# Optimization experiments

Hardware: AMD Instinct MI355X
Metric: run time of the kernel (lower is better)

The kernel has to match this reference:

```python
import jax, jax.numpy as jnp
import numpy as np

N_NODES = 500000
N_EDGES = 16000000


def setup_inputs() -> dict:
    key = jax.random.key(0)
    k1, k2, k3, k4, k5, k6, k7 = jax.random.split(key, 7)
    x = jax.random.normal(k1, (N_NODES, 2), dtype=jnp.float32)
    edge_index = jax.random.randint(k2, (2, N_EDGES), 0, N_NODES, dtype=jnp.int64)
    edge_weight = jax.random.uniform(k3, (N_EDGES,), dtype=jnp.float32)
    # GCNConv linear weights (PyG stores weight [in, out] for x @ W) + bias
    W1 = jax.random.normal(k4, (2, 8), dtype=jnp.float32) * (1.0 / np.sqrt(2.0))
    b1 = jnp.zeros((8,), dtype=jnp.float32)
    W2 = jax.random.normal(k5, (8, 2), dtype=jnp.float32) * (1.0 / np.sqrt(8.0))
    b2 = jnp.zeros((2,), dtype=jnp.float32)
    return {"x": x, "edge_index": edge_index, "edge_weight": edge_weight,
            "W1": W1, "b1": b1, "W2": W2, "b2": b2}


def _gcn_norm(edge_index, edge_weight, num_nodes):
    # PyG gcn_norm: add self-loops (fill=1), symmetric D^-1/2 A D^-1/2
    loop = jnp.arange(num_nodes, dtype=edge_index.dtype)
    src = jnp.concatenate([edge_index[0], loop])
    dst = jnp.concatenate([edge_index[1], loop])
    w = jnp.concatenate([edge_weight, jnp.ones((num_nodes,), edge_weight.dtype)])
    deg = jax.ops.segment_sum(w, dst, num_segments=num_nodes)
    dinv = jnp.where(deg > 0, jax.lax.rsqrt(jnp.where(deg > 0, deg, 1.0)), 0.0)
    norm = dinv[src] * w * dinv[dst]
    return src, dst, norm


def _gcn_layer(x, src, dst, norm, W, b, num_nodes):
    h = x @ W                      # [N, out]
    msg = h[src] * norm[:, None]   # gather + edge scale, [E+N, out]
    out = jax.ops.segment_sum(msg, dst, num_segments=num_nodes)  # scatter-add
    return out + b


def reference(x, edge_index, edge_weight, W1, b1, W2, b2):
    n = x.shape[0]
    src, dst, norm = _gcn_norm(edge_index, edge_weight, n)
    h = _gcn_layer(x, src, dst, norm, W1, b1, n)
    h = jax.nn.relu(h)
    h = _gcn_layer(h, src, dst, norm, W2, b2, n)
    return jax.nn.softmax(h, axis=1)
```

## Files before the change

kernel.cpp:

```cpp
#include <hip/hip_runtime.h>
#include <math.h>

#define NNODES 500000
#define NEDGES 16000000
#define NBINS 512
#define BINSHIFT 10
#define BINMASK 1023
#define CB 512
#define NT 256


#define OFF_FLAG   0
#define OFF_BASE   64
#define OFF_TOT    1024
#define OFF_COUNTS 2048
#define OFF_OFFS   264192
#define OFF_DEGREP 526336
#define OFF_DINV   1526336
#define OFF_AGG1   2026336
#define OFF_AGG2   4026336
#define OFF_H2     6026336
#define OFF_REC    7026336
#define WS_NEED_FAST (((size_t)OFF_REC + 2ull * NEDGES) * 4ull)

__device__ __forceinline__ void atomAddF(float* p, float v) {
    unsafeAtomicAdd(p, v);
}

__device__ __forceinline__ int clampIdx(int i) {
    return ((unsigned)i < (unsigned)NNODES) ? i : 0;
}

template <bool I64>
__device__ __forceinline__ int4 loadIdx4(const int* __restrict__ p, int i) {
    if (!I64) {
        return ((const int4*)p)[i];
    } else {
        const longlong2* q = (const longlong2*)p;
        longlong2 a = q[2 * i];
        longlong2 b = q[2 * i + 1];
        return make_int4((int)a.x, (int)a.y, (int)b.x, (int)b.y);
    }
}

__global__ __launch_bounds__(256) void k_detect(
        const int* __restrict__ ei, int* __restrict__ flag) {
    __shared__ int any_nz;
    if (threadIdx.x == 0) any_nz = 0;
    __syncthreads();
    int nz = 0;
    const int SAMPLES = 1024;
    const int step = NEDGES / SAMPLES;
    for (int t = threadIdx.x; t < SAMPLES; t += blockDim.x) {
        int k = t * step;
        nz |= (ei[2 * k + 1] != 0);
    }
    if (nz) atomicOr(&any_nz, 1);
    __syncthreads();
    if (threadIdx.x == 0) flag[0] = any_nz ? 0 : 1;
}


template <bool I64>
__device__ __forceinline__ void count_body(
        const int* __restrict__ dstb, unsigned* __restrict__ counts) {
    __shared__ unsigned hist[NBINS];
    for (int j = threadIdx.x; j < NBINS; j += NT) hist[j] = 0;
    __syncthreads();
    const int Q = NEDGES / 4;
    const int qpb = (Q + CB - 1) / CB;
    int q0 = blockIdx.x * qpb, q1 = min(q0 + qpb, Q);
    for (int i = q0 + threadIdx.x; i < q1; i += NT) {
        int4 d = loadIdx4<I64>(dstb, i);
        atomicAdd(&hist[clampIdx(d.x) >> BINSHIFT], 1u);
        atomicAdd(&hist[clampIdx(d.y) >> BINSHIFT], 1u);
        atomicAdd(&hist[clampIdx(d.z) >> BINSHIFT], 1u);
        atomicAdd(&hist[clampIdx(d.w) >> BINSHIFT], 1u);
    }
    __syncthreads();
    for (int j = threadIdx.x; j < NBINS; j += NT)
        counts[(size_t)j * CB + blockIdx.x] = hist[j];
}

__global__ __launch_bounds__(256) void kb_count(
        const int* __restrict__ ei, const int* __restrict__ flag,
        unsigned* __restrict__ counts) {
    if (flag[0]) count_body<true >(ei + 2 * (size_t)NEDGES, counts);
    else         count_body<false>(ei + (size_t)NEDGES,     counts);
}

__global__ __launch_bounds__(256) void kb_tot(
        const unsigned* __restrict__ counts, unsigned* __restrict__ tot) {
    int b = blockIdx.x, t = threadIdx.x;
    __shared__ unsigned r[NT];
    r[t] = counts[(size_t)b * CB + t] + counts[(size_t)b * CB + t + 256];
    __syncthreads();
    for (int d = NT / 2; d > 0; d >>= 1) {
        if (t < d) r[t] += r[t + d];
        __syncthreads();
    }
    if (t == 0) tot[b] = r[0];
}

__global__ __launch_bounds__(256) void kb_scanbase(
        const unsigned* __restrict__ tot, unsigned* __restrict__ base) {
    __shared__ unsigned sc[NBINS];
    int t = threadIdx.x;
    unsigned o0 = tot[t], o1 = tot[t + 256];
    sc[t] = o0; sc[t + 256] = o1;
    __syncthreads();
    for (int d = 1; d < NBINS; d <<= 1) {
        unsigned a0 = (t >= d) ? sc[t - d] : 0u;
        unsigned a1 = (t + 256 >= d) ? sc[t + 256 - d] : 0u;
        __syncthreads();
        sc[t] += a0; sc[t + 256] += a1;
        __syncthreads();
    }
    base[t] = sc[t] - o0;
    base[t + 256] = sc[t + 256] - o1;
    if (t == 255) base[NBINS] = sc[NBINS - 1];
}

__global__ __launch_bounds__(256) void kb_offsets(
        const unsigned* __restrict__ counts, const unsigned* __restrict__ base,
        unsigned* __restrict__ offs) {
    int b = blockIdx.x, t = threadIdx.x;
    __shared__ unsigned sc[CB];
    unsigned o0 = counts[(size_t)b * CB + t], o1 = counts[(size_t)b * CB + t + 256];
    sc[t] = o0; sc[t + 256] = o1;
    __syncthreads();
    for (int d = 1; d < CB; d <<= 1) {
        unsigned a0 = (t >= d) ? sc[t - d] : 0u;
        unsigned a1 = (t + 256 >= d) ? sc[t + 256 - d] : 0u;
        __syncthreads();
        sc[t] += a0; sc[t + 256] += a1;
        __syncthreads();
    }
    unsigned bb = base[b];
    offs[(size_t)b * CB + t]       = bb + sc[t] - o0;
    offs[(size_t)b * CB + t + 256] = bb + sc[t + 256] - o1;
}

template <bool I64>
__device__ __forceinline__ void scatter_body(
        const int* __restrict__ srcb, const int* __restrict__ dstb,
        const float* __restrict__ ew, const unsigned* __restrict__ offs,
        uint2* __restrict__ rec) {
    __shared__ unsigned cur[NBINS];
    for (int j = threadIdx.x; j < NBINS; j += NT)
        cur[j] = offs[(size_t)j * CB + blockIdx.x];
    __syncthreads();
    const int Q = NEDGES / 4;
    const int qpb = (Q + CB - 1) / CB;
    int q0 = blockIdx.x * qpb, q1 = min(q0 + qpb, Q);
    for (int i = q0 + threadIdx.x; i < q1; i += NT) {
        int4   s = loadIdx4<I64>(srcb, i);
        int4   d = loadIdx4<I64>(dstb, i);
        float4 w = ((const float4*)ew)[i];
        int sv[4] = {clampIdx(s.x), clampIdx(s.y), clampIdx(s.z), clampIdx(s.w)};
        int dv[4] = {clampIdx(d.x), clampIdx(d.y), clampIdx(d.z), clampIdx(d.w)};
        float wv[4] = {w.x, w.y, w.z, w.w};
#pragma unroll
        for (int k = 0; k < 4; ++k) {
            int bin = dv[k] >> BINSHIFT;
            unsigned slot = atomicAdd(&cur[bin], 1u);
            unsigned key = ((unsigned)(dv[k] & BINMASK) << 19) | (unsigned)sv[k];
            rec[slot] = make_uint2(key, __float_as_uint(wv[k]));
        }
    }
}

__global__ __launch_bounds__(256) void kb_scatter(
        const int* __restrict__ ei, const int* __restrict__ flag,
        const float* __restrict__ ew, const unsigned* __restrict__ offs,
        uint2* __restrict__ rec) {
    if (flag[0]) scatter_body<true >(ei, ei + 2 * (size_t)NEDGES, ew, offs, rec);
    else         scatter_body<false>(ei, ei + (size_t)NEDGES,     ew, offs, rec);
}

__global__ __launch_bounds__(256) void kb_degree(
        const uint2* __restrict__ rec, const unsigned* __restrict__ base,
        float* __restrict__ degrep) {
    int bin = blockIdx.x >> 1, half = blockIdx.x & 1, t = threadIdx.x;
    __shared__ float sdeg[1024];
    for (int j = t; j < 1024; j += NT) sdeg[j] = 0.f;
    __syncthreads();
    int s = base[bin], e = base[bin + 1];
    int len = e - s, h = len >> 1;
    int b0 = s + (half ? h : 0);
    int b1 = half ? e : s + h;
    for (int i = b0 + t; i < b1; i += NT) {
        uint2 r = rec[i];
        atomAddF(&sdeg[r.x >> 19], __uint_as_float(r.y));
    }
    __syncthreads();
    int nodebase = bin << BINSHIFT;
    for (int j = t; j < 1024; j += NT) {
        int node = nodebase + j;
        if (node < NNODES) degrep[(size_t)half * NNODES + node] = sdeg[j];
    }
}

__global__ __launch_bounds__(256) void kb_dinv(
        const float* __restrict__ degrep, float* __restrict__ dinv, int N) {
    int i = blockIdx.x * blockDim.x + threadIdx.x;
    if (i >= N) return;
    dinv[i] = rsqrtf(degrep[i] + degrep[(size_t)N + i] + 1.0f);
}

__global__ __launch_bounds__(256) void kb_agg(
        const uint2* __restrict__ rec, const unsigned* __restrict__ base,
        const float* __restrict__ dinv, const float2* __restrict__ feat,
        float2* __restrict__ outrep) {
    int bin = blockIdx.x >> 1, half = blockIdx.x & 1, t = threadIdx.x;
    __shared__ float sagg[2048];
    __shared__ float sdinv[1024];
    for (int j = t; j < 2048; j += NT) sagg[j] = 0.f;
    int nodebase = bin << BINSHIFT;
    for (int j = t; j < 1024; j += NT) {
        int node = nodebase + j;
        sdinv[j] = (node < NNODES) ? dinv[node] : 0.f;
    }
    __syncthreads();
    int s = base[bin], e = base[bin + 1];
    int len = e - s, h = len >> 1;
    int b0 = s + (half ? h : 0);
    int b1 = half ? e : s + h;
    for (int i = b0 + t; i < b1; i += NT) {
        uint2 r = rec[i];
        int dl  = r.x >> 19;
        int src = r.x & 0x7FFFF;
        float nrm = dinv[src] * __uint_as_float(r.y) * sdinv[dl];
        float2 f = feat[src];
        atomAddF(&sagg[2 * dl],     f.x * nrm);
        atomAddF(&sagg[2 * dl + 1], f.y * nrm);
    }
    __syncthreads();
    for (int j = t; j < 1024; j += NT) {
        int node = nodebase + j;
        if (node < NNODES)
            outrep[(size_t)half * NNODES + node] = make_float2(sagg[2 * j], sagg[2 * j + 1]);
    }
}

__global__ __launch_bounds__(256) void kb_mid(
        const float2* __restrict__ aggrep, const float2* __restrict__ x,
        const float* __restrict__ dinv, const float* __restrict__ W1,
        const float* __restrict__ b1, const float* __restrict__ W2,
        float2* __restrict__ h2, int N) {
    int i = blockIdx.x * blockDim.x + threadIdx.x;
    if (i >= N) return;
    float s = dinv[i], s2 = s * s;
    float2 a0 = aggrep[i], a1 = aggrep[(size_t)N + i];
    float2 xa = x[i];
    float vx = a0.x + a1.x + xa.x * s2;
    float vy = a0.y + a1.y + xa.y * s2;
    float o0 = 0.f, o1 = 0.f;
#pragma unroll
    for (int j = 0; j < 8; ++j) {
        float tt = fmaf(vx, W1[j], fmaf(vy, W1[8 + j], b1[j]));
        tt = fmaxf(tt, 0.0f);
        o0 = fmaf(tt, W2[2 * j],     o0);
        o1 = fmaf(tt, W2[2 * j + 1], o1);
    }
    h2[i] = make_float2(o0, o1);
}

__global__ __launch_bounds__(256) void kb_fin(
        const float2* __restrict__ aggrep, const float2* __restrict__ h2,
        const float* __restrict__ dinv, const float* __restrict__ b2,
        float2* __restrict__ out, int N) {
    int i = blockIdx.x * blockDim.x + threadIdx.x;
    if (i >= N) return;
    float s = dinv[i], s2 = s * s;
    float2 a0 = aggrep[i], a1 = aggrep[(size_t)N + i];
    float2 h = h2[i];
    float o0 = a0.x + a1.x + h.x * s2 + b2[0];
    float o1 = a0.y + a1.y + h.y * s2 + b2[1];
    float m  = fmaxf(o0, o1);
    float e0 = expf(o0 - m), e1 = expf(o1 - m);
    float inv = 1.0f / (e0 + e1);
    out[i] = make_float2(e0 * inv, e1 * inv);
}


__global__ __launch_bounds__(256) void k_zero(float4* __restrict__ p, int n4) {
    int stride = gridDim.x * blockDim.x;
    for (int i = blockIdx.x * blockDim.x + threadIdx.x; i < n4; i += stride)
        p[i] = make_float4(0.f, 0.f, 0.f, 0.f);
}

template <bool I64>
__device__ __forceinline__ void degree_body(
        const int* __restrict__ dst, const float* __restrict__ ew,
        float* __restrict__ deg, int Q) {
    int stride = gridDim.x * blockDim.x;
    for (int i = blockIdx.x * blockDim.x + threadIdx.x; i < Q; i += stride) {
        int4   d = loadIdx4<I64>(dst, i);
        float4 w = ((const float4*)ew)[i];
        atomAddF(&deg[clampIdx(d.x)], w.x);
        atomAddF(&deg[clampIdx(d.y)], w.y);
        atomAddF(&deg[clampIdx(d.z)], w.z);
        atomAddF(&deg[clampIdx(d.w)], w.w);
    }
}

__global__ __launch_bounds__(256) void k_degree(
        const int* __restrict__ ei, const int* __restrict__ flag,
        const float* __restrict__ ew, float* __restrict__ deg, int Q) {
    if (flag[0]) degree_body<true >(ei + 2 * (size_t)NEDGES, ew, deg, Q);
    else         degree_body<false>(ei + (size_t)NEDGES,     ew, deg, Q);
}

__global__ __launch_bounds__(256) void k_dinv(float* __restrict__ deg, int N) {
    int i = blockIdx.x * blockDim.x + threadIdx.x;
    if (i >= N) return;
    deg[i] = rsqrtf(deg[i] + 1.0f);
}

template <bool I64>
__device__ __forceinline__ void edge_body(
        const int* __restrict__ src, const int* __restrict__ dst,
        const float* __restrict__ ew, const float* __restrict__ dinv,
        const float* __restrict__ feat, float* __restrict__ agg, int Q) {
    int stride = gridDim.x * blockDim.x;
    for (int i = blockIdx.x * blockDim.x + threadIdx.x; i < Q; i += stride) {
        int4   s = loadIdx4<I64>(src, i);
        int4   d = loadIdx4<I64>(dst, i);
        float4 w = ((const float4*)ew)[i];
        s.x = clampIdx(s.x); s.y = clampIdx(s.y);
        s.z = clampIdx(s.z); s.w = clampIdx(s.w);
        d.x = clampIdx(d.x); d.y = clampIdx(d.y);
        d.z = clampIdx(d.z); d.w = clampIdx(d.w);
        float n0 = dinv[s.x] * w.x * dinv[d.x];
        float n1 = dinv[s.y] * w.y * dinv[d.y];
        float n2 = dinv[s.z] * w.z * dinv[d.z];
        float n3 = dinv[s.w] * w.w * dinv[d.w];
        float2 f0 = ((const float2*)feat)[s.x];
        float2 f1 = ((const float2*)feat)[s.y];
        float2 f2 = ((const float2*)feat)[s.z];
        float2 f3 = ((const float2*)feat)[s.w];
        float* o0 = agg + 2 * (size_t)d.x;
        float* o1 = agg + 2 * (size_t)d.y;
        float* o2 = agg + 2 * (size_t)d.z;
        float* o3 = agg + 2 * (size_t)d.w;
        atomAddF(o0,     f0.x * n0);
        atomAddF(o0 + 1, f0.y * n0);
        atomAddF(o1,     f1.x * n1);
        atomAddF(o1 + 1, f1.y * n1);
        atomAddF(o2,     f2.x * n2);
        atomAddF(o2 + 1, f2.y * n2);
        atomAddF(o3,     f3.x * n3);
        atomAddF(o3 + 1, f3.y * n3);
    }
}

__global__ __launch_bounds__(256) void k_edge(
        const int* __restrict__ ei, const int* __restrict__ flag,
        const float* __restrict__ ew, const float* __restrict__ dinv,
        const float* __restrict__ feat, float* __restrict__ agg, int Q) {
    if (flag[0]) edge_body<true >(ei, ei + 2 * (size_t)NEDGES, ew, dinv, feat, agg, Q);
    else         edge_body<false>(ei, ei + (size_t)NEDGES,     ew, dinv, feat, agg, Q);
}

__global__ __launch_bounds__(256) void k_mid(
        const float* __restrict__ aggX, const float* __restrict__ x,
        const float* __restrict__ dinv, const float* __restrict__ W1,
        const float* __restrict__ b1, const float* __restrict__ W2,
        float* __restrict__ h2, int N) {
    int i = blockIdx.x * blockDim.x + threadIdx.x;
    if (i >= N) return;
    float s = dinv[i], s2 = s * s;
    float2 xa = ((const float2*)x)[i];
    float2 ag = ((const float2*)aggX)[i];
    float vx = ag.x + xa.x * s2;
    float vy = ag.y + xa.y * s2;
    float o0 = 0.f, o1 = 0.f;
#pragma unroll
    for (int j = 0; j < 8; ++j) {
        float t = fmaf(vx, W1[j], fmaf(vy, W1[8 + j], b1[j]));
        t = fmaxf(t, 0.0f);
        o0 = fmaf(t, W2[2 * j],     o0);
        o1 = fmaf(t, W2[2 * j + 1], o1);
    }
    ((float2*)h2)[i] = make_float2(o0, o1);
}

__global__ __launch_bounds__(256) void k_fin(
        const float* __restrict__ agg2, const float* __restrict__ h2,
        const float* __restrict__ dinv, const float* __restrict__ b2,
        float* __restrict__ out, int N) {
    int i = blockIdx.x * blockDim.x + threadIdx.x;
    if (i >= N) return;
    float s = dinv[i], s2 = s * s;
    float2 a = ((const float2*)agg2)[i];
    float2 h = ((const float2*)h2)[i];
    float o0 = a.x + h.x * s2 + b2[0];
    float o1 = a.y + h.y * s2 + b2[1];
    float m  = fmaxf(o0, o1);
    float e0 = expf(o0 - m), e1 = expf(o1 - m);
    float inv = 1.0f / (e0 + e1);
    ((float2*)out)[i] = make_float2(e0 * inv, e1 * inv);
}


extern "C" void kernel_launch(void* const* d_in, const int* in_sizes, int n_in,
                              void* d_out, int out_size, void* d_ws, size_t ws_size,
                              hipStream_t stream) {
    const float* x  = (const float*)d_in[0];
    const int*   ei = (const int*)d_in[1];
    const float* ew = (const float*)d_in[2];
    const float* W1 = (const float*)d_in[3];
    const float* b1 = (const float*)d_in[4];
    const float* W2 = (const float*)d_in[5];
    const float* b2 = (const float*)d_in[6];
    float* out = (float*)d_out;
    unsigned* wsu = (unsigned*)d_ws;
    float*    wsf = (float*)d_ws;

    const int N = NNODES, E = NEDGES, Q = E / 4;
    const int NB = (N + NT - 1) / NT;
    int* flag = (int*)(wsu + OFF_FLAG);

    bool fast = ws_size >= WS_NEED_FAST;

    k_detect<<<1, NT, 0, stream>>>(ei, flag);

    if (fast) {
        unsigned* base   = wsu + OFF_BASE;
        unsigned* tot    = wsu + OFF_TOT;
        unsigned* counts = wsu + OFF_COUNTS;
        unsigned* offs   = wsu + OFF_OFFS;
        float*    degrep = wsf + OFF_DEGREP;
        float*    dinv   = wsf + OFF_DINV;
        float2*   agg1   = (float2*)(wsf + OFF_AGG1);
        float2*   agg2   = (float2*)(wsf + OFF_AGG2);
        float2*   h2     = (float2*)(wsf + OFF_H2);
        uint2*    rec    = (uint2*)(wsu + OFF_REC);

        kb_count   <<<CB,        NT, 0, stream>>>(ei, flag, counts);
        kb_tot     <<<NBINS,     NT, 0, stream>>>(counts, tot);
        kb_scanbase<<<1,         NT, 0, stream>>>(tot, base);
        kb_offsets <<<NBINS,     NT, 0, stream>>>(counts, base, offs);
        kb_scatter <<<CB,        NT, 0, stream>>>(ei, flag, ew, offs, rec);
        kb_degree  <<<2 * NBINS, NT, 0, stream>>>(rec, base, degrep);
        kb_dinv    <<<NB,        NT, 0, stream>>>(degrep, dinv, N);
        kb_agg     <<<2 * NBINS, NT, 0, stream>>>(rec, base, dinv, (const float2*)x, agg1);
        kb_mid     <<<NB,        NT, 0, stream>>>(agg1, (const float2*)x, dinv, W1, b1, W2, h2, N);
        kb_agg     <<<2 * NBINS, NT, 0, stream>>>(rec, base, dinv, (const float2*)h2, agg2);
        kb_fin     <<<NB,        NT, 0, stream>>>(agg2, h2, dinv, b2, (float2*)out, N);
    } else {
        float* deg  = wsf + 64;
        float* aggX = wsf + 64 + (size_t)N;
        float* agg2 = wsf + 64 + (size_t)3 * N;
        float* h2   = wsf + 64 + (size_t)5 * N;
        const int EB = 2048;
        const int ZB = ((5 * N / 4) + NT - 1) / NT;

        k_zero  <<<ZB, NT, 0, stream>>>((float4*)deg, 5 * N / 4);
        k_degree<<<EB, NT, 0, stream>>>(ei, flag, ew, deg, Q);
        k_dinv  <<<NB, NT, 0, stream>>>(deg, N);
        k_edge  <<<EB, NT, 0, stream>>>(ei, flag, ew, deg, x, aggX, Q);
        k_mid   <<<NB, NT, 0, stream>>>(aggX, x, deg, W1, b1, W2, h2, N);
        k_edge  <<<EB, NT, 0, stream>>>(ei, flag, ew, deg, h2, agg2, Q);
        k_fin   <<<NB, NT, 0, stream>>>(agg2, h2, deg, b2, out, N);
    }
}
```

Before: 921.0 us.

## Use larger destination bins, four-way replication, and non-temporal edge loads

Destination bins grow from 1024 to 2048 nodes, giving 256 bins, with 1024 count blocks. Each bin is now split across four replica blocks instead of two, and the count and offset matrices are stored block-major, which changes the scan kernels. The destination dinv factor moves out of the per-edge loop into the mid and final kernels, and edge streams use non-temporal loads. The aim is more parallel blocks per bin, fewer per-edge multiplies, and less cache pollution, at the cost of twice the replica partial buffers to read and reduce per node.

```diff
diff --git a/kernel.cpp b/kernel.cpp
--- a/kernel.cpp
+++ b/kernel.cpp
@@ -3,10 +3,11 @@
 
 #define NNODES 500000
 #define NEDGES 16000000
-#define NBINS 512
-#define BINSHIFT 10
-#define BINMASK 1023
-#define CB 512
+#define NBINS 256
+#define BINSHIFT 11
+#define BINMASK 2047
+#define CB 1024
+#define REP 4
 #define NT 256
 
 
@@ -16,12 +17,15 @@
 #define OFF_COUNTS 2048
 #define OFF_OFFS   264192
 #define OFF_DEGREP 526336
-#define OFF_DINV   1526336
-#define OFF_AGG1   2026336
-#define OFF_AGG2   4026336
-#define OFF_H2     6026336
+#define OFF_H2     526336
+#define OFF_DINV   2526336
+#define OFF_AGG    3026336
 #define OFF_REC    7026336
 #define WS_NEED_FAST (((size_t)OFF_REC + 2ull * NEDGES) * 4ull)
+
+typedef int       i32x4 __attribute__((ext_vector_type(4)));
+typedef float     f32x4 __attribute__((ext_vector_type(4)));
+typedef long long i64x2 __attribute__((ext_vector_type(2)));
 
 __device__ __forceinline__ void atomAddF(float* p, float v) {
     unsafeAtomicAdd(p, v);
@@ -43,6 +47,23 @@
     }
 }
 
+template <bool I64>
+__device__ __forceinline__ int4 loadIdx4NT(const int* __restrict__ p, int i) {
+    if (!I64) {
+        i32x4 v = __builtin_nontemporal_load(((const i32x4*)p) + i);
+        return make_int4(v.x, v.y, v.z, v.w);
+    } else {
+        i64x2 a = __builtin_nontemporal_load(((const i64x2*)p) + 2 * i);
+        i64x2 b = __builtin_nontemporal_load(((const i64x2*)p) + 2 * i + 1);
+        return make_int4((int)a.x, (int)a.y, (int)b.x, (int)b.y);
+    }
+}
+
+__device__ __forceinline__ float4 loadF4NT(const float* __restrict__ p, int i) {
+    f32x4 v = __builtin_nontemporal_load(((const f32x4*)p) + i);
+    return make_float4(v.x, v.y, v.z, v.w);
+}
+
 __global__ __launch_bounds__(256) void k_detect(
         const int* __restrict__ ei, int* __restrict__ flag) {
     __shared__ int any_nz;
@@ -71,7 +92,7 @@
     const int qpb = (Q + CB - 1) / CB;
     int q0 = blockIdx.x * qpb, q1 = min(q0 + qpb, Q);
     for (int i = q0 + threadIdx.x; i < q1; i += NT) {
-        int4 d = loadIdx4<I64>(dstb, i);
+        int4 d = loadIdx4NT<I64>(dstb, i);
         atomicAdd(&hist[clampIdx(d.x) >> BINSHIFT], 1u);
         atomicAdd(&hist[clampIdx(d.y) >> BINSHIFT], 1u);
         atomicAdd(&hist[clampIdx(d.z) >> BINSHIFT], 1u);
@@ -79,7 +100,7 @@
     }
     __syncthreads();
     for (int j = threadIdx.x; j < NBINS; j += NT)
-        counts[(size_t)j * CB + blockIdx.x] = hist[j];
+        counts[(size_t)blockIdx.x * NBINS + j] = hist[j];
 }
 
 __global__ __launch_bounds__(256) void kb_count(
@@ -91,54 +112,65 @@
 
 __global__ __launch_bounds__(256) void kb_tot(
         const unsigned* __restrict__ counts, unsigned* __restrict__ tot) {
-    int b = blockIdx.x, t = threadIdx.x;
+    int j = blockIdx.x, t = threadIdx.x;
     __shared__ unsigned r[NT];
-    r[t] = counts[(size_t)b * CB + t] + counts[(size_t)b * CB + t + 256];
+    unsigned s = 0;
+#pragma unroll
+    for (int k = 0; k < CB / NT; ++k)
+        s += counts[(size_t)(t * (CB / NT) + k) * NBINS + j];
+    r[t] = s;
     __syncthreads();
     for (int d = NT / 2; d > 0; d >>= 1) {
         if (t < d) r[t] += r[t + d];
         __syncthreads();
     }
-    if (t == 0) tot[b] = r[0];
+    if (t == 0) tot[j] = r[0];
 }
 
 __global__ __launch_bounds__(256) void kb_scanbase(
         const unsigned* __restrict__ tot, unsigned* __restrict__ base) {
     __shared__ unsigned sc[NBINS];
     int t = threadIdx.x;
-    unsigned o0 = tot[t], o1 = tot[t + 256];
-    sc[t] = o0; sc[t + 256] = o1;
+    unsigned o = tot[t];
+    sc[t] = o;
     __syncthreads();
     for (int d = 1; d < NBINS; d <<= 1) {
-        unsigned a0 = (t >= d) ? sc[t - d] : 0u;
-        unsigned a1 = (t + 256 >= d) ? sc[t + 256 - d] : 0u;
+        unsigned a = (t >= d) ? sc[t - d] : 0u;
         __syncthreads();
-        sc[t] += a0; sc[t + 256] += a1;
+        sc[t] += a;
         __syncthreads();
     }
-    base[t] = sc[t] - o0;
-    base[t + 256] = sc[t + 256] - o1;
-    if (t == 255) base[NBINS] = sc[NBINS - 1];
+    base[t] = sc[t] - o;
+    if (t == NBINS - 1) base[NBINS] = sc[NBINS - 1];
 }
 
 __global__ __launch_bounds__(256) void kb_offsets(
         const unsigned* __restrict__ counts, const unsigned* __restrict__ base,
         unsigned* __restrict__ offs) {
-    int b = blockIdx.x, t = threadIdx.x;
-    __shared__ unsigned sc[CB];
-    unsigned o0 = counts[(size_t)b * CB + t], o1 = counts[(size_t)b * CB + t + 256];
-    sc[t] = o0; sc[t + 256] = o1;
-    __syncthreads();
-    for (int d = 1; d < CB; d <<= 1) {
-        unsigned a0 = (t >= d) ? sc[t - d] : 0u;
-        unsigned a1 = (t + 256 >= d) ? sc[t + 256 - d] : 0u;
+    int j = blockIdx.x, t = threadIdx.x;
+    const int K = CB / NT;
+    __shared__ unsigned part[NT];
+    unsigned loc[K];
+    unsigned s = 0;
+#pragma unroll
+    for (int k = 0; k < K; ++k) {
+        loc[k] = counts[(size_t)(t * K + k) * NBINS + j];
+        s += loc[k];
+    }
+    part[t] = s;
+    __syncthreads();
+    for (int d = 1; d < NT; d <<= 1) {
+        unsigned a = (t >= d) ? part[t - d] : 0u;
         __syncthreads();
-        sc[t] += a0; sc[t + 256] += a1;
+        part[t] += a;
         __syncthreads();
     }
-    unsigned bb = base[b];
-    offs[(size_t)b * CB + t]       = bb + sc[t] - o0;
-    offs[(size_t)b * CB + t + 256] = bb + sc[t + 256] - o1;
+    unsigned run = base[j] + part[t] - s;
+#pragma unroll
+    for (int k = 0; k < K; ++k) {
+        offs[(size_t)(t * K + k) * NBINS + j] = run;
+        run += loc[k];
+    }
 }
 
 template <bool I64>
@@ -148,15 +180,15 @@
         uint2* __restrict__ rec) {
     __shared__ unsigned cur[NBINS];
     for (int j = threadIdx.x; j < NBINS; j += NT)
-        cur[j] = offs[(size_t)j * CB + blockIdx.x];
+        cur[j] = offs[(size_t)blockIdx.x * NBINS + j];
     __syncthreads();
     const int Q = NEDGES / 4;
     const int qpb = (Q + CB - 1) / CB;
     int q0 = blockIdx.x * qpb, q1 = min(q0 + qpb, Q);
     for (int i = q0 + threadIdx.x; i < q1; i += NT) {
-        int4   s = loadIdx4<I64>(srcb, i);
-        int4   d = loadIdx4<I64>(dstb, i);
-        float4 w = ((const float4*)ew)[i];
+        int4   s = loadIdx4NT<I64>(srcb, i);
+        int4   d = loadIdx4NT<I64>(dstb, i);
+        float4 w = loadF4NT(ew, i);
         int sv[4] = {clampIdx(s.x), clampIdx(s.y), clampIdx(s.z), clampIdx(s.w)};
         int dv[4] = {clampIdx(d.x), clampIdx(d.y), clampIdx(d.z), clampIdx(d.w)};
         float wv[4] = {w.x, w.y, w.z, w.w};
@@ -181,23 +213,23 @@
 __global__ __launch_bounds__(256) void kb_degree(
         const uint2* __restrict__ rec, const unsigned* __restrict__ base,
         float* __restrict__ degrep) {
-    int bin = blockIdx.x >> 1, half = blockIdx.x & 1, t = threadIdx.x;
-    __shared__ float sdeg[1024];
-    for (int j = t; j < 1024; j += NT) sdeg[j] = 0.f;
+    int bin = blockIdx.x >> 2, r = blockIdx.x & (REP - 1), t = threadIdx.x;
+    __shared__ float sdeg[1 << BINSHIFT];
+    for (int j = t; j < (1 << BINSHIFT); j += NT) sdeg[j] = 0.f;
     __syncthreads();
     int s = base[bin], e = base[bin + 1];
-    int len = e - s, h = len >> 1;
-    int b0 = s + (half ? h : 0);
-    int b1 = half ? e : s + h;
+    int len = e - s;
+    int b0 = s + (len * r) / REP;
+    int b1 = s + (len * (r + 1)) / REP;
     for (int i = b0 + t; i < b1; i += NT) {
-        uint2 r = rec[i];
-        atomAddF(&sdeg[r.x >> 19], __uint_as_float(r.y));
+        uint2 rr = rec[i];
+        atomAddF(&sdeg[rr.x >> 19], __uint_as_float(rr.y));
     }
     __syncthreads();
     int nodebase = bin << BINSHIFT;
-    for (int j = t; j < 1024; j += NT) {
+    for (int j = t; j < (1 << BINSHIFT); j += NT) {
         int node = nodebase + j;
-        if (node < NNODES) degrep[(size_t)half * NNODES + node] = sdeg[j];
+        if (node < NNODES) degrep[(size_t)r * NNODES + node] = sdeg[j];
     }
 }
 
@@ -205,41 +237,38 @@
         const float* __restrict__ degrep, float* __restrict__ dinv, int N) {
     int i = blockIdx.x * blockDim.x + threadIdx.x;
     if (i >= N) return;
-    dinv[i] = rsqrtf(degrep[i] + degrep[(size_t)N + i] + 1.0f);
+    float d = degrep[i] + degrep[(size_t)N + i]
+            + degrep[2 * (size_t)N + i] + degrep[3 * (size_t)N + i];
+    dinv[i] = rsqrtf(d + 1.0f);
 }
 
 __global__ __launch_bounds__(256) void kb_agg(
         const uint2* __restrict__ rec, const unsigned* __restrict__ base,
         const float* __restrict__ dinv, const float2* __restrict__ feat,
         float2* __restrict__ outrep) {
-    int bin = blockIdx.x >> 1, half = blockIdx.x & 1, t = threadIdx.x;
-    __shared__ float sagg[2048];
-    __shared__ float sdinv[1024];
-    for (int j = t; j < 2048; j += NT) sagg[j] = 0.f;
-    int nodebase = bin << BINSHIFT;
-    for (int j = t; j < 1024; j += NT) {
-        int node = nodebase + j;
-        sdinv[j] = (node < NNODES) ? dinv[node] : 0.f;
-    }
+    int bin = blockIdx.x >> 2, r = blockIdx.x & (REP - 1), t = threadIdx.x;
+    __shared__ float sagg[2 << BINSHIFT];
+    for (int j = t; j < (2 << BINSHIFT); j += NT) sagg[j] = 0.f;
     __syncthreads();
     int s = base[bin], e = base[bin + 1];
-    int len = e - s, h = len >> 1;
-    int b0 = s + (half ? h : 0);
-    int b1 = half ? e : s + h;
+    int len = e - s;
+    int b0 = s + (len * r) / REP;
+    int b1 = s + (len * (r + 1)) / REP;
     for (int i = b0 + t; i < b1; i += NT) {
-        uint2 r = rec[i];
-        int dl  = r.x >> 19;
-        int src = r.x & 0x7FFFF;
-        float nrm = dinv[src] * __uint_as_float(r.y) * sdinv[dl];
+        uint2 rr = rec[i];
+        int dl  = rr.x >> 19;
+        int src = rr.x & 0x7FFFF;
+        float nrm = dinv[src] * __uint_as_float(rr.y);
         float2 f = feat[src];
         atomAddF(&sagg[2 * dl],     f.x * nrm);
         atomAddF(&sagg[2 * dl + 1], f.y * nrm);
     }
     __syncthreads();
-    for (int j = t; j < 1024; j += NT) {
+    int nodebase = bin << BINSHIFT;
+    for (int j = t; j < (1 << BINSHIFT); j += NT) {
         int node = nodebase + j;
         if (node < NNODES)
-            outrep[(size_t)half * NNODES + node] = make_float2(sagg[2 * j], sagg[2 * j + 1]);
+            outrep[(size_t)r * NNODES + node] = make_float2(sagg[2 * j], sagg[2 * j + 1]);
     }
 }
 
@@ -251,10 +280,11 @@
     int i = blockIdx.x * blockDim.x + threadIdx.x;
     if (i >= N) return;
     float s = dinv[i], s2 = s * s;
-    float2 a0 = aggrep[i], a1 = aggrep[(size_t)N + i];
+    float2 a0 = aggrep[i],                 a1 = aggrep[(size_t)N + i];
+    float2 a2 = aggrep[2 * (size_t)N + i], a3 = aggrep[3 * (size_t)N + i];
     float2 xa = x[i];
-    float vx = a0.x + a1.x + xa.x * s2;
-    float vy = a0.y + a1.y + xa.y * s2;
+    float vx = s * (a0.x + a1.x + a2.x + a3.x) + xa.x * s2;
+    float vy = s * (a0.y + a1.y + a2.y + a3.y) + xa.y * s2;
     float o0 = 0.f, o1 = 0.f;
 #pragma unroll
     for (int j = 0; j < 8; ++j) {
@@ -273,10 +303,11 @@
     int i = blockIdx.x * blockDim.x + threadIdx.x;
     if (i >= N) return;
     float s = dinv[i], s2 = s * s;
-    float2 a0 = aggrep[i], a1 = aggrep[(size_t)N + i];
+    float2 a0 = aggrep[i],                 a1 = aggrep[(size_t)N + i];
+    float2 a2 = aggrep[2 * (size_t)N + i], a3 = aggrep[3 * (size_t)N + i];
     float2 h = h2[i];
-    float o0 = a0.x + a1.x + h.x * s2 + b2[0];
-    float o1 = a0.y + a1.y + h.y * s2 + b2[1];
+    float o0 = s * (a0.x + a1.x + a2.x + a3.x) + h.x * s2 + b2[0];
+    float o1 = s * (a0.y + a1.y + a2.y + a3.y) + h.y * s2 + b2[1];
     float m  = fmaxf(o0, o1);
     float e0 = expf(o0 - m), e1 = expf(o1 - m);
     float inv = 1.0f / (e0 + e1);
@@ -433,22 +464,21 @@
         unsigned* offs   = wsu + OFF_OFFS;
         float*    degrep = wsf + OFF_DEGREP;
         float*    dinv   = wsf + OFF_DINV;
-        float2*   agg1   = (float2*)(wsf + OFF_AGG1);
-        float2*   agg2   = (float2*)(wsf + OFF_AGG2);
+        float2*   agg    = (float2*)(wsf + OFF_AGG);
         float2*   h2     = (float2*)(wsf + OFF_H2);
         uint2*    rec    = (uint2*)(wsu + OFF_REC);
 
-        kb_count   <<<CB,        NT, 0, stream>>>(ei, flag, counts);
-        kb_tot     <<<NBINS,     NT, 0, stream>>>(counts, tot);
-        kb_scanbase<<<1,         NT, 0, stream>>>(tot, base);
-        kb_offsets <<<NBINS,     NT, 0, stream>>>(counts, base, offs);
-        kb_scatter <<<CB,        NT, 0, stream>>>(ei, flag, ew, offs, rec);
-        kb_degree  <<<2 * NBINS, NT, 0, stream>>>(rec, base, degrep);
-        kb_dinv    <<<NB,        NT, 0, stream>>>(degrep, dinv, N);
-        kb_agg     <<<2 * NBINS, NT, 0, stream>>>(rec, base, dinv, (const float2*)x, agg1);
-        kb_mid     <<<NB,        NT, 0, stream>>>(agg1, (const float2*)x, dinv, W1, b1, W2, h2, N);
-        kb_agg     <<<2 * NBINS, NT, 0, stream>>>(rec, base, dinv, (const float2*)h2, agg2);
-        kb_fin     <<<NB,        NT, 0, stream>>>(agg2, h2, dinv, b2, (float2*)out, N);
+        kb_count   <<<CB,          NT, 0, stream>>>(ei, flag, counts);
+        kb_tot     <<<NBINS,       NT, 0, stream>>>(counts, tot);
+        kb_scanbase<<<1,           NT, 0, stream>>>(tot, base);
+        kb_offsets <<<NBINS,       NT, 0, stream>>>(counts, base, offs);
+        kb_scatter <<<CB,          NT, 0, stream>>>(ei, flag, ew, offs, rec);
+        kb_degree  <<<NBINS * REP, NT, 0, stream>>>(rec, base, degrep);
+        kb_dinv    <<<NB,          NT, 0, stream>>>(degrep, dinv, N);
+        kb_agg     <<<NBINS * REP, NT, 0, stream>>>(rec, base, dinv, (const float2*)x, agg);
+        kb_mid     <<<NB,          NT, 0, stream>>>(agg, (const float2*)x, dinv, W1, b1, W2, h2, N);
+        kb_agg     <<<NBINS * REP, NT, 0, stream>>>(rec, base, dinv, (const float2*)h2, agg);
+        kb_fin     <<<NB,          NT, 0, stream>>>(agg, h2, dinv, b2, (float2*)out, N);
     } else {
         float* deg  = wsf + 64;
         float* aggX = wsf + 64 + (size_t)N;
```

After: 879.5 us. 1.05x faster.
